# Performance work log

Hardware: AMD Instinct MI355X
Metric: run time of the kernel (lower is better)

Reference implementation:

```python
import jax, jax.numpy as jnp
import numpy as np
import math

D_MODEL = 1024
N_HEAD = 16
B, T = 4, 2048


def setup_inputs() -> dict:
    key = jax.random.key(0)
    ks = jax.random.split(key, 12)
    s = 1.0 / math.sqrt(D_MODEL)
    inp = {
        "q": jax.random.normal(ks[0], (B, T, D_MODEL), dtype=jnp.float32),
        "k": jax.random.normal(ks[1], (B, T, D_MODEL), dtype=jnp.float32),
        "v": jax.random.normal(ks[2], (B, T, D_MODEL), dtype=jnp.float32),
        "Wq": jax.random.uniform(ks[3], (D_MODEL, D_MODEL), jnp.float32, -s, s),
        "bq": jax.random.uniform(ks[4], (D_MODEL,), jnp.float32, -s, s),
        "Wk": jax.random.uniform(ks[5], (D_MODEL, D_MODEL), jnp.float32, -s, s),
        "bk": jax.random.uniform(ks[6], (D_MODEL,), jnp.float32, -s, s),
        "Wv": jax.random.uniform(ks[7], (D_MODEL, D_MODEL), jnp.float32, -s, s),
        "bv": jax.random.uniform(ks[8], (D_MODEL,), jnp.float32, -s, s),
        "Wo": jax.random.uniform(ks[9], (D_MODEL, D_MODEL), jnp.float32, -s, s),
        "bo": jax.random.uniform(ks[10], (D_MODEL,), jnp.float32, -s, s),
    }
    return inp


def reference(q, k, v, Wq, bq, Wk, bk, Wv, bv, Wo, bo):
    # NOTE: original module applies all three projections to `q` (k, v args unused)
    batch, time, dim = q.shape
    n_d = dim // N_HEAD
    # torch Linear: x @ W.T + b
    Q = (q @ Wq.T + bq).reshape(batch, time, N_HEAD, n_d).transpose(0, 2, 1, 3)
    K = (q @ Wk.T + bk).reshape(batch, time, N_HEAD, n_d).transpose(0, 2, 1, 3)
    V = (q @ Wv.T + bv).reshape(batch, time, N_HEAD, n_d).transpose(0, 2, 1, 3)
    # [B, H, T, T]
    score = jnp.einsum("bhqd,bhkd->bhqk", Q, K) / jnp.sqrt(jnp.float32(n_d))
    causal = jnp.tril(jnp.ones((time, time), dtype=bool))
    score = jnp.where(causal, score, -jnp.inf)
    # original uses Softmax(dim=-2): normalizes over the QUERY axis (faithful)
    attn = jax.nn.softmax(score, axis=-2)
    ctx = jnp.einsum("bhqk,bhkd->bhqd", attn, V)
    ctx = ctx.transpose(0, 2, 1, 3).reshape(batch, time, dim)
    return ctx @ Wo.T + bo
```

## Files before the change

### kernel.cpp

```cpp
#include <hip/hip_runtime.h>
#include <hip/hip_bf16.h>
#include <cstdint>
#include <cstddef>

typedef __bf16 bf16x8 __attribute__((ext_vector_type(8)));
typedef __bf16 bf16x4 __attribute__((ext_vector_type(4)));
typedef __bf16 bf16x2 __attribute__((ext_vector_type(2)));
typedef float  f32x4  __attribute__((ext_vector_type(4)));

static constexpr int TSEQ  = 2048;
static constexpr int DM    = 1024;
static constexpr int NH    = 16;
static constexpr int HD    = 64;
static constexpr int BATCH = 4;
static constexpr float SCL = 0.18033688011112042f;

__device__ __forceinline__ void gload16(const __bf16* g, __bf16* l) {
  __builtin_amdgcn_global_load_lds((const __attribute__((address_space(1))) void*)g,
                                   (__attribute__((address_space(3))) void*)l, 16, 0, 0);
}

#define PBAR()  asm volatile("s_barrier" ::: "memory")
#define LGKM()  asm volatile("s_waitcnt lgkmcnt(0)" ::: "memory")

__global__ __launch_bounds__(256) void cvt_kernel(const float* __restrict__ in,
                                                  __bf16* __restrict__ out, int n4) {
  int i = blockIdx.x * 256 + threadIdx.x;
  if (i < n4) {
    float4 v = reinterpret_cast<const float4*>(in)[i];
    bf16x4 o;
    o[0] = (__bf16)v.x; o[1] = (__bf16)v.y; o[2] = (__bf16)v.z; o[3] = (__bf16)v.w;
    reinterpret_cast<bf16x4*>(out)[i] = o;
  }
}

__global__ __launch_bounds__(256) void cvt4_kernel(
    const float* __restrict__ a, const float* __restrict__ bsrc,
    const float* __restrict__ c, const float* __restrict__ d,
    __bf16* __restrict__ oa, __bf16* __restrict__ ob,
    __bf16* __restrict__ oc, __bf16* __restrict__ od, int n4) {
  const float* src = (blockIdx.y == 0) ? a : (blockIdx.y == 1) ? bsrc
                    : (blockIdx.y == 2) ? c : d;
  __bf16* dst = (blockIdx.y == 0) ? oa : (blockIdx.y == 1) ? ob
               : (blockIdx.y == 2) ? oc : od;
  int i = blockIdx.x * 256 + threadIdx.x;
  if (i < n4) {
    float4 v = reinterpret_cast<const float4*>(src)[i];
    bf16x4 o;
    o[0] = (__bf16)v.x; o[1] = (__bf16)v.y; o[2] = (__bf16)v.z; o[3] = (__bf16)v.w;
    reinterpret_cast<bf16x4*>(dst)[i] = o;
  }
}

__global__ __launch_bounds__(512, 2) void gemm_qkv_kernel(
    const __bf16* __restrict__ A, const __bf16* __restrict__ Wqkv,
    const float* __restrict__ b0, const float* __restrict__ b1,
    const float* __restrict__ b2, __bf16* __restrict__ QKVp) {
  __shared__ __align__(16) __bf16 lA[2 * 256 * 64];
  __shared__ __align__(16) __bf16 lB[2 * 192 * 64];
  const int flat = blockIdx.x;
  const int xcd = flat & 7, idx = flat >> 3;
  const int mi = xcd * 4 + (idx & 3);
  const int nig = idx >> 2;
  const int i0 = mi * 256, o0 = nig * 192;

  const int tid = threadIdx.x;
  const int l = tid & 63, lr = l & 15, lg = l >> 4;
  const int w = tid >> 6;
  const int wr = w >> 2, wc = w & 3;

  f32x4 acc[8][3];
  const f32x4 fzero = {0.f, 0.f, 0.f, 0.f};
#pragma unroll
  for (int mm = 0; mm < 8; ++mm)
#pragma unroll
    for (int ni = 0; ni < 3; ++ni) acc[mm][ni] = fzero;

  const int s_row = tid >> 3;
  const int s_cc  = tid & 7;
  const __bf16* Ab = A + (size_t)i0 * DM;
  const __bf16* Wb = Wqkv + (size_t)o0 * DM;

  auto stageA = [&](int buf, int kt, int h) {
#pragma unroll
    for (int rr = 0; rr < 2; ++rr) {
      int row = h * 128 + rr * 64 + s_row;
      gload16(Ab + (size_t)row * DM + kt * 64 + ((s_cc ^ (row & 7)) << 3),
              lA + buf * 16384 + (h * 128 + rr * 64) * 64 + tid * 8);
    }
  };
  auto stageB = [&](int buf, int kt, int n) {
    int row = n * 64 + s_row;
    gload16(Wb + (size_t)row * DM + kt * 64 + ((s_cc ^ (row & 7)) << 3),
            lB + buf * 12288 + n * 4096 + tid * 8);
  };
  auto rdA = [&](const __bf16* base, int row, int ks) {
    int chunk = (ks * 4 + lg) ^ (row & 7);
    return *(const bf16x8*)(base + row * 64 + chunk * 8);
  };

  const int NT = DM / 64;

#pragma unroll
  for (int h = 0; h < 2; ++h) stageA(0, 0, h);
#pragma unroll
  for (int n = 0; n < 3; ++n) stageB(0, 0, n);
#pragma unroll
  for (int h = 0; h < 2; ++h) stageA(1, 1, h);
#pragma unroll
  for (int n = 0; n < 3; ++n) stageB(1, 1, n);
  asm volatile("s_waitcnt vmcnt(7)" ::: "memory");
  PBAR();

  for (int t = 0; t < NT; ++t) {
    const int cur = t & 1;
    const __bf16* cA = lA + cur * 16384;
    const __bf16* cB = lB + cur * 12288;
    const bool pre = (t + 2 < NT);

    bf16x8 afl[4][2], afh[4][2], bfl[2][2], bfh[1][2];

#pragma unroll
    for (int mm = 0; mm < 4; ++mm)
#pragma unroll
      for (int ks = 0; ks < 2; ++ks)
        afl[mm][ks] = rdA(cA, wr * 128 + mm * 16 + lr, ks);
#pragma unroll
    for (int ni = 0; ni < 2; ++ni)
#pragma unroll
      for (int ks = 0; ks < 2; ++ks)
        bfl[ni][ks] = rdA(cB, wc * 48 + ni * 16 + lr, ks);
    PBAR(); LGKM();
    __builtin_amdgcn_s_setprio(1);
#pragma unroll
    for (int mm = 0; mm < 4; ++mm)
#pragma unroll
      for (int ni = 0; ni < 2; ++ni)
#pragma unroll
        for (int ks = 0; ks < 2; ++ks)
          acc[mm][ni] = __builtin_amdgcn_mfma_f32_16x16x32_bf16(
              afl[mm][ks], bfl[ni][ks], acc[mm][ni], 0, 0, 0);
    __builtin_amdgcn_s_setprio(0);
    PBAR();

#pragma unroll
    for (int ks = 0; ks < 2; ++ks)
      bfh[0][ks] = rdA(cB, wc * 48 + 2 * 16 + lr, ks);
    if (pre) { stageB(cur, t + 2, 0); stageB(cur, t + 2, 1); }
    PBAR(); LGKM();
    __builtin_amdgcn_s_setprio(1);
#pragma unroll
    for (int mm = 0; mm < 4; ++mm)
#pragma unroll
      for (int ks = 0; ks < 2; ++ks)
        acc[mm][2] = __builtin_amdgcn_mfma_f32_16x16x32_bf16(
            afl[mm][ks], bfh[0][ks], acc[mm][2], 0, 0, 0);
    __builtin_amdgcn_s_setprio(0);
    PBAR();

#pragma unroll
    for (int mm = 0; mm < 4; ++mm)
#pragma unroll
      for (int ks = 0; ks < 2; ++ks)
        afh[mm][ks] = rdA(cA, wr * 128 + (mm + 4) * 16 + lr, ks);
    if (pre) { stageB(cur, t + 2, 2); stageA(cur, t + 2, 0); }
    PBAR(); LGKM();
    __builtin_amdgcn_s_setprio(1);
#pragma unroll
    for (int mm = 0; mm < 4; ++mm)
#pragma unroll
      for (int ni = 0; ni < 2; ++ni)
#pragma unroll
        for (int ks = 0; ks < 2; ++ks)
          acc[mm + 4][ni] = __builtin_amdgcn_mfma_f32_16x16x32_bf16(
              afh[mm][ks], bfl[ni][ks], acc[mm + 4][ni], 0, 0, 0);
    __builtin_amdgcn_s_setprio(0);
    PBAR();

    if (pre) stageA(cur, t + 2, 1);
    if (pre)                asm volatile("s_waitcnt vmcnt(7)" ::: "memory");
    else if (t + 1 < NT)    asm volatile("s_waitcnt vmcnt(0)" ::: "memory");
    PBAR();
    __builtin_amdgcn_s_setprio(1);
#pragma unroll
    for (int mm = 0; mm < 4; ++mm)
#pragma unroll
      for (int ks = 0; ks < 2; ++ks)
        acc[mm + 4][2] = __builtin_amdgcn_mfma_f32_16x16x32_bf16(
            afh[mm][ks], bfh[0][ks], acc[mm + 4][2], 0, 0, 0);
    __builtin_amdgcn_s_setprio(0);
    PBAR();
  }

#pragma unroll
  for (int ni = 0; ni < 3; ++ni) {
    int col = o0 + wc * 48 + ni * 16 + lr;
    int z = col >> 10, cin = col & 1023;
    const float* bp = (z == 0) ? b0 : (z == 1) ? b1 : b2;
    float bb = bp[cin];
    __bf16* O = QKVp + (size_t)z * 8192 * DM;
#pragma unroll
    for (int mm = 0; mm < 8; ++mm) {
      int row = i0 + wr * 128 + mm * 16 + lg * 4;
#pragma unroll
      for (int r = 0; r < 4; ++r)
        O[(size_t)(row + r) * DM + cin] = (__bf16)(acc[mm][ni][r] + bb);
    }
  }
}

template <typename OUT_T>
__device__ __forceinline__ void gemm_body2(
    const __bf16* __restrict__ A, const __bf16* __restrict__ W,
    const float* __restrict__ bias, OUT_T* __restrict__ C,
    int i0, int o0, __bf16* lA, __bf16* lB) {
  const int tid = threadIdx.x;
  const int l = tid & 63, lr = l & 15, lg = l >> 4;
  const int w = tid >> 6;
  const int wr = w >> 2, wc = w & 3;

  f32x4 acc[4][4];
  const f32x4 fzero = {0.f, 0.f, 0.f, 0.f};
#pragma unroll
  for (int mi = 0; mi < 4; ++mi)
#pragma unroll
    for (int ni = 0; ni < 4; ++ni) acc[mi][ni] = fzero;

  const int s_row = tid >> 3;
  const int s_cc  = tid & 7;
  const int NT = DM / 64;

  {
#pragma unroll
    for (int n = 0; n < 2; ++n) {
      int row = n * 64 + s_row;
      gload16(A + (size_t)(i0 + row) * DM + ((s_cc ^ (row & 7)) << 3),
              lA + n * 4096 + tid * 8);
    }
#pragma unroll
    for (int n = 0; n < 4; ++n) {
      int row = n * 64 + s_row;
      gload16(W + (size_t)(o0 + row) * DM + ((s_cc ^ (row & 7)) << 3),
              lB + n * 4096 + tid * 8);
    }
  }
  asm volatile("s_waitcnt vmcnt(0)" ::: "memory");
  __syncthreads();

  for (int t = 0; t < NT; ++t) {
    const int cur = t & 1;
    if (t + 1 < NT) {
      const int k0 = (t + 1) * 64;
      const int nxt = cur ^ 1;
#pragma unroll
      for (int n = 0; n < 2; ++n) {
        int row = n * 64 + s_row;
        gload16(A + (size_t)(i0 + row) * DM + k0 + ((s_cc ^ (row & 7)) << 3),
                lA + nxt * 8192 + n * 4096 + tid * 8);
      }
#pragma unroll
      for (int n = 0; n < 4; ++n) {
        int row = n * 64 + s_row;
        gload16(W + (size_t)(o0 + row) * DM + k0 + ((s_cc ^ (row & 7)) << 3),
                lB + nxt * 16384 + n * 4096 + tid * 8);
      }
    }

    const __bf16* cA = lA + cur * 8192;
    const __bf16* cB = lB + cur * 16384;

    bf16x8 af[4][2], bf_[2][2];
#pragma unroll
    for (int mi = 0; mi < 4; ++mi)
#pragma unroll
      for (int ks = 0; ks < 2; ++ks) {
        int row = wr * 64 + mi * 16 + lr;
        int chunk = (ks * 4 + lg) ^ (row & 7);
        af[mi][ks] = *(const bf16x8*)(cA + row * 64 + chunk * 8);
      }
#pragma unroll
    for (int ni = 0; ni < 2; ++ni)
#pragma unroll
      for (int ks = 0; ks < 2; ++ks) {
        int row = wc * 64 + ni * 16 + lr;
        int chunk = (ks * 4 + lg) ^ (row & 7);
        bf_[ni][ks] = *(const bf16x8*)(cB + row * 64 + chunk * 8);
      }
    __builtin_amdgcn_s_setprio(1);
#pragma unroll
    for (int mi = 0; mi < 4; ++mi)
#pragma unroll
      for (int ni = 0; ni < 2; ++ni)
#pragma unroll
        for (int ks = 0; ks < 2; ++ks)
          acc[mi][ni] = __builtin_amdgcn_mfma_f32_16x16x32_bf16(
              af[mi][ks], bf_[ni][ks], acc[mi][ni], 0, 0, 0);
    __builtin_amdgcn_s_setprio(0);

#pragma unroll
    for (int ni = 0; ni < 2; ++ni)
#pragma unroll
      for (int ks = 0; ks < 2; ++ks) {
        int row = wc * 64 + (ni + 2) * 16 + lr;
        int chunk = (ks * 4 + lg) ^ (row & 7);
        bf_[ni][ks] = *(const bf16x8*)(cB + row * 64 + chunk * 8);
      }
    __builtin_amdgcn_s_setprio(1);
#pragma unroll
    for (int mi = 0; mi < 4; ++mi)
#pragma unroll
      for (int ni = 0; ni < 2; ++ni)
#pragma unroll
        for (int ks = 0; ks < 2; ++ks)
          acc[mi][ni + 2] = __builtin_amdgcn_mfma_f32_16x16x32_bf16(
              af[mi][ks], bf_[ni][ks], acc[mi][ni + 2], 0, 0, 0);
    __builtin_amdgcn_s_setprio(0);

    if (t + 1 < NT) {
      asm volatile("s_waitcnt vmcnt(0)" ::: "memory");
      __syncthreads();
    }
  }

#pragma unroll
  for (int ni = 0; ni < 4; ++ni) {
    int col = o0 + wc * 64 + ni * 16 + lr;
    float bb = bias[col];
#pragma unroll
    for (int mi = 0; mi < 4; ++mi) {
      int row = i0 + wr * 64 + mi * 16 + lg * 4;
#pragma unroll
      for (int r = 0; r < 4; ++r)
        C[(size_t)(row + r) * DM + col] = (OUT_T)(acc[mi][ni][r] + bb);
    }
  }
}

__global__ __launch_bounds__(512, 2) void gemm_out_kernel(
    const __bf16* __restrict__ A, const __bf16* __restrict__ W,
    const float* __restrict__ bias, float* __restrict__ C) {
  __shared__ __align__(16) __bf16 lA[2 * 128 * 64];
  __shared__ __align__(16) __bf16 lB[2 * 256 * 64];
  const int flat = blockIdx.x;
  const int xcd = flat & 7, idx = flat >> 3;
  const int mi = xcd * 8 + (idx & 7);
  const int ni = idx >> 3;
  gemm_body2<float>(A, W, bias, C, mi * 128, ni * 256, lA, lB);
}

__global__ __launch_bounds__(256) void colstats_kernel(
    const __bf16* __restrict__ Q, const __bf16* __restrict__ K,
    const __bf16* __restrict__ V, __bf16* __restrict__ VT) {
  const int flat = blockIdx.x;
  const int wid = (flat & 7) * 128 + (flat >> 3);
  const int g = wid >> 4, bx = wid & 15;
  const int h = g & 15, b = g >> 4;
  const int tid = threadIdx.x;
  const int w = tid >> 6, l = tid & 63, lr = l & 15, lg = l >> 4;
  const size_t base = (size_t)b * TSEQ * DM + (size_t)h * HD;

  __shared__ float part[4][64];
  __shared__ float invc[64];

  for (int ph = 0; ph < 2; ++ph) {
    const int kt = ph ? (31 - bx) : bx;
    const int k0 = kt * 64;

    bf16x8 kf[4][2];
#pragma unroll
    for (int ct = 0; ct < 4; ++ct)
#pragma unroll
      for (int ks = 0; ks < 2; ++ks)
        kf[ct][ks] = *(const bf16x8*)(K + base + (size_t)(k0 + ct * 16 + lr) * DM +
                                      ks * 32 + lg * 8);

    float csum[4] = {0.f, 0.f, 0.f, 0.f};
    const int nchunks = (TSEQ - k0) >> 4;
    for (int jj = w; jj < nchunks; jj += 4) {
      int qrow = k0 + jj * 16;
      bf16x8 a0 = *(const bf16x8*)(Q + base + (size_t)(qrow + lr) * DM + lg * 8);
      bf16x8 a1 = *(const bf16x8*)(Q + base + (size_t)(qrow + lr) * DM + 32 + lg * 8);
      const bool interior = (jj >= 4);
#pragma unroll
      for (int ct = 0; ct < 4; ++ct) {
        f32x4 s = {0.f, 0.f, 0.f, 0.f};
        s = __builtin_amdgcn_mfma_f32_16x16x32_bf16(a0, kf[ct][0], s, 0, 0, 0);
        s = __builtin_amdgcn_mfma_f32_16x16x32_bf16(a1, kf[ct][1], s, 0, 0, 0);
        if (interior) {
#pragma unroll
          for (int r = 0; r < 4; ++r) csum[ct] += __builtin_amdgcn_exp2f(s[r] * SCL);
        } else {
#pragma unroll
          for (int r = 0; r < 4; ++r) {
            int ql = jj * 16 + lg * 4 + r;
            int kl = ct * 16 + lr;
            float e = __builtin_amdgcn_exp2f(s[r] * SCL);
            csum[ct] += (ql >= kl) ? e : 0.f;
          }
        }
      }
    }

#pragma unroll
    for (int ct = 0; ct < 4; ++ct) {
      csum[ct] += __shfl_xor(csum[ct], 16, 64);
      csum[ct] += __shfl_xor(csum[ct], 32, 64);
    }

    if (l < 16) {
#pragma unroll
      for (int ct = 0; ct < 4; ++ct) part[w][ct * 16 + l] = csum[ct];
    }
    __syncthreads();
    if (tid < 64) {
      float c = part[0][tid] + part[1][tid] + part[2][tid] + part[3][tid];
      invc[tid] = 1.0f / c;
    }
    __syncthreads();

    const int d = tid >> 2, gq = tid & 3;
    size_t vtb = (((size_t)(b * NH + h)) * HD + d) * TSEQ + k0 + gq * 16;
#pragma unroll
    for (int kc = 0; kc < 16; kc += 2) {
      int kl = gq * 16 + kc;
      float v0 = (float)V[base + (size_t)(k0 + kl) * DM + d] * invc[kl];
      float v1 = (float)V[base + (size_t)(k0 + kl + 1) * DM + d] * invc[kl + 1];
      bf16x2 o; o[0] = (__bf16)v0; o[1] = (__bf16)v1;
      *(bf16x2*)(VT + vtb + kc) = o;
    }
    __syncthreads();
  }
}

__device__ __forceinline__ int swz(int e) { return e ^ (((e >> 6) & 7) << 3); }

__global__ __launch_bounds__(256, 4) void ctx_kernel(
    const __bf16* __restrict__ Q, const __bf16* __restrict__ K,
    const __bf16* __restrict__ VT, __bf16* __restrict__ CTX) {
  __shared__ __align__(16) __bf16 lK[4096];
  __shared__ __align__(16) __bf16 lV[4096];
  __shared__ __align__(16) __bf16 lP[8][16 * 88];
  const int flat = blockIdx.x;
  const int wid = (flat & 7) * 128 + (flat >> 3);
  const int g = wid >> 4, bx = wid & 15;
  const int h = g & 15, b = g >> 4;
  const int tid = threadIdx.x;
  const int w = tid >> 6, l = tid & 63, lr = l & 15, lg = l >> 4;
  const size_t base = (size_t)b * TSEQ * DM + (size_t)h * HD;
  const size_t vtb = ((size_t)(b * NH + h)) * HD * TSEQ;
  __bf16* pw1 = &lP[w][0];
  __bf16* pw2 = &lP[w + 4][0];

  const int qt1 = 31 - bx, qt2 = bx;
  const int q01 = qt1 * 64, q02 = qt2 * 64;

  const int srow = w * 8 + (l >> 3);
  const int scol = (((l & 7) ^ (l >> 3)) << 3);

  bf16x8 qf1[2], qf2[2];
#pragma unroll
  for (int ks = 0; ks < 2; ++ks) {
    qf1[ks] = *(const bf16x8*)(Q + base + (size_t)(q01 + w * 16 + lr) * DM + ks * 32 + lg * 8);
    qf2[ks] = *(const bf16x8*)(Q + base + (size_t)(q02 + w * 16 + lr) * DM + ks * 32 + lg * 8);
  }

  f32x4 acc1[4], acc2[4];
  const f32x4 fzero = {0.f, 0.f, 0.f, 0.f};
#pragma unroll
  for (int dt = 0; dt < 4; ++dt) { acc1[dt] = fzero; acc2[dt] = fzero; }

  for (int kt = 0; kt <= qt1; ++kt) {
    const int k0 = kt * 64;
    const bool two = (kt <= qt2);
    __syncthreads();
#pragma unroll
    for (int n = 0; n < 2; ++n) {
      gload16(K + base + (size_t)(k0 + n * 32 + srow) * DM + scol,
              lK + n * 2048 + w * 512);
      gload16(VT + vtb + (size_t)(n * 32 + srow) * TSEQ + k0 + scol,
              lV + n * 2048 + w * 512);
    }
    asm volatile("s_waitcnt vmcnt(0)" ::: "memory");
    __syncthreads();

    const bool diag1 = (kt == qt1), diag2 = (kt == qt2);
#pragma unroll
    for (int ct = 0; ct < 4; ++ct) {
      bf16x8 kb[2];
#pragma unroll
      for (int ks = 0; ks < 2; ++ks) {
        int e = (ct * 16 + lr) * 64 + ks * 32 + lg * 8;
        kb[ks] = *(const bf16x8*)(lK + swz(e));
      }
      {
        f32x4 s = {0.f, 0.f, 0.f, 0.f};
        s = __builtin_amdgcn_mfma_f32_16x16x32_bf16(kb[0], qf1[0], s, 0, 0, 0);
        s = __builtin_amdgcn_mfma_f32_16x16x32_bf16(kb[1], qf1[1], s, 0, 0, 0);
        bf16x4 pk;
        if (diag1) {
#pragma unroll
          for (int r = 0; r < 4; ++r) {
            int ql = w * 16 + lr, kl = ct * 16 + lg * 4 + r;
            pk[r] = (__bf16)((ql >= kl) ? __builtin_amdgcn_exp2f(s[r] * SCL) : 0.f);
          }
        } else {
#pragma unroll
          for (int r = 0; r < 4; ++r)
            pk[r] = (__bf16)__builtin_amdgcn_exp2f(s[r] * SCL);
        }
        *(bf16x4*)(pw1 + lr * 88 + ct * 16 + lg * 4) = pk;
      }
      if (two) {
        f32x4 s = {0.f, 0.f, 0.f, 0.f};
        s = __builtin_amdgcn_mfma_f32_16x16x32_bf16(kb[0], qf2[0], s, 0, 0, 0);
        s = __builtin_amdgcn_mfma_f32_16x16x32_bf16(kb[1], qf2[1], s, 0, 0, 0);
        bf16x4 pk;
        if (diag2) {
#pragma unroll
          for (int r = 0; r < 4; ++r) {
            int ql = w * 16 + lr, kl = ct * 16 + lg * 4 + r;
            pk[r] = (__bf16)((ql >= kl) ? __builtin_amdgcn_exp2f(s[r] * SCL) : 0.f);
          }
        } else {
#pragma unroll
          for (int r = 0; r < 4; ++r)
            pk[r] = (__bf16)__builtin_amdgcn_exp2f(s[r] * SCL);
        }
        *(bf16x4*)(pw2 + lr * 88 + ct * 16 + lg * 4) = pk;
      }
    }
    asm volatile("" ::: "memory");

    bf16x8 pa1[2], pa2[2];
#pragma unroll
    for (int ks = 0; ks < 2; ++ks)
      pa1[ks] = *(const bf16x8*)(pw1 + lr * 88 + ks * 32 + lg * 8);
    if (two) {
#pragma unroll
      for (int ks = 0; ks < 2; ++ks)
        pa2[ks] = *(const bf16x8*)(pw2 + lr * 88 + ks * 32 + lg * 8);
    }
#pragma unroll
    for (int dt = 0; dt < 4; ++dt) {
#pragma unroll
      for (int ks = 0; ks < 2; ++ks) {
        int e = (dt * 16 + lr) * 64 + ks * 32 + lg * 8;
        bf16x8 vb8 = *(const bf16x8*)(lV + swz(e));
        acc1[dt] = __builtin_amdgcn_mfma_f32_16x16x32_bf16(pa1[ks], vb8, acc1[dt], 0, 0, 0);
        if (two)
          acc2[dt] = __builtin_amdgcn_mfma_f32_16x16x32_bf16(pa2[ks], vb8, acc2[dt], 0, 0, 0);
      }
    }
  }

#pragma unroll
  for (int dt = 0; dt < 4; ++dt)
#pragma unroll
    for (int r = 0; r < 4; ++r) {
      CTX[base + (size_t)(q01 + w * 16 + lg * 4 + r) * DM + dt * 16 + lr] = (__bf16)acc1[dt][r];
      CTX[base + (size_t)(q02 + w * 16 + lg * 4 + r) * DM + dt * 16 + lr] = (__bf16)acc2[dt][r];
    }
}

extern "C" void kernel_launch(void* const* d_in, const int* in_sizes, int n_in,
                              void* d_out, int out_size, void* d_ws, size_t ws_size,
                              hipStream_t stream) {
  const float* q  = (const float*)d_in[0];
  const float* Wq = (const float*)d_in[3];
  const float* bq = (const float*)d_in[4];
  const float* Wk = (const float*)d_in[5];
  const float* bk = (const float*)d_in[6];
  const float* Wv = (const float*)d_in[7];
  const float* bv = (const float*)d_in[8];
  const float* Wo = (const float*)d_in[9];
  const float* bo = (const float*)d_in[10];
  float* out = (float*)d_out;

  const size_t NTOK = (size_t)BATCH * TSEQ;
  char* ws = (char*)d_ws;
  __bf16* qb   = (__bf16*)ws; ws += NTOK * DM * 2;
  __bf16* Wqkv = (__bf16*)ws; ws += 3 * (size_t)DM * DM * 2;
  __bf16* Wob  = (__bf16*)ws; ws += (size_t)DM * DM * 2;
  __bf16* QKVp = (__bf16*)ws; ws += 3 * NTOK * DM * 2;
  __bf16* VT   = (__bf16*)ws; ws += (size_t)BATCH * NH * HD * TSEQ * 2;
  __bf16* CTX = qb;

  __bf16* Qp = QKVp;
  __bf16* Kp = QKVp + NTOK * DM;
  __bf16* Vp = QKVp + 2 * NTOK * DM;

  const int nq4 = (int)(NTOK * DM / 4);
  const int nw4 = DM * DM / 4;
  cvt_kernel<<<(nq4 + 255) / 256, 256, 0, stream>>>(q, qb, nq4);
  cvt4_kernel<<<dim3((nw4 + 255) / 256, 4), 256, 0, stream>>>(
      Wq, Wk, Wv, Wo, Wqkv, Wqkv + (size_t)DM * DM, Wqkv + 2 * (size_t)DM * DM, Wob, nw4);

  gemm_qkv_kernel<<<512, 512, 0, stream>>>(qb, Wqkv, bq, bk, bv, QKVp);

  colstats_kernel<<<1024, 256, 0, stream>>>(Qp, Kp, Vp, VT);
  ctx_kernel<<<1024, 256, 0, stream>>>(Qp, Kp, VT, CTX);

  gemm_out_kernel<<<256, 512, 0, stream>>>(CTX, Wob, bo, out);
}
```

Measured before the change: 209.1 us.

## Prefetch next-tile LDS fragments in QKV GEMM and fuse colstats key-tile phases

The QKV GEMM main loop now loads the next tile's A/B low fragments from LDS at the end of each iteration, and moves the afh loads earlier. It uses partial lgkmcnt waits so LDS reads overlap with MFMA work instead of stalling at full waits. The colstats kernel handles both key tiles (bx and 31-bx) in one pass over Q rows, so each Q fragment is loaded once and shared by both tiles' score sums. This costs more registers (two K fragment sets, persistent fragment arrays) and could reduce occupancy.

```diff
diff --git a/kernel.cpp b/kernel.cpp
--- a/kernel.cpp
+++ b/kernel.cpp
@@ -20,8 +20,8 @@
                                    (__attribute__((address_space(3))) void*)l, 16, 0, 0);
 }
 
-#define PBAR()  asm volatile("s_barrier" ::: "memory")
-#define LGKM()  asm volatile("s_waitcnt lgkmcnt(0)" ::: "memory")
+#define PBAR()   asm volatile("s_barrier" ::: "memory")
+#define LGKMN(n) asm volatile("s_waitcnt lgkmcnt(" #n ")" ::: "memory")
 
 __global__ __launch_bounds__(256) void cvt_kernel(const float* __restrict__ in,
                                                   __bf16* __restrict__ out, int n4) {
@@ -112,25 +112,31 @@
   asm volatile("s_waitcnt vmcnt(7)" ::: "memory");
   PBAR();
 
+  bf16x8 afl[4][2], afh[4][2], bfl[2][2], bfh[2];
+#pragma unroll
+  for (int mm = 0; mm < 4; ++mm)
+#pragma unroll
+    for (int ks = 0; ks < 2; ++ks)
+      afl[mm][ks] = rdA(lA, wr * 128 + mm * 16 + lr, ks);
+#pragma unroll
+  for (int ni = 0; ni < 2; ++ni)
+#pragma unroll
+    for (int ks = 0; ks < 2; ++ks)
+      bfl[ni][ks] = rdA(lB, wc * 48 + ni * 16 + lr, ks);
+
   for (int t = 0; t < NT; ++t) {
     const int cur = t & 1;
     const __bf16* cA = lA + cur * 16384;
     const __bf16* cB = lB + cur * 12288;
+    const __bf16* nA = lA + (cur ^ 1) * 16384;
+    const __bf16* nB = lB + (cur ^ 1) * 12288;
     const bool pre = (t + 2 < NT);
-
-    bf16x8 afl[4][2], afh[4][2], bfl[2][2], bfh[1][2];
-
-#pragma unroll
-    for (int mm = 0; mm < 4; ++mm)
-#pragma unroll
-      for (int ks = 0; ks < 2; ++ks)
-        afl[mm][ks] = rdA(cA, wr * 128 + mm * 16 + lr, ks);
-#pragma unroll
-    for (int ni = 0; ni < 2; ++ni)
-#pragma unroll
-      for (int ks = 0; ks < 2; ++ks)
-        bfl[ni][ks] = rdA(cB, wc * 48 + ni * 16 + lr, ks);
-    PBAR(); LGKM();
+    const bool hasnext = (t + 1 < NT);
+
+#pragma unroll
+    for (int ks = 0; ks < 2; ++ks)
+      bfh[ks] = rdA(cB, wc * 48 + 2 * 16 + lr, ks);
+    PBAR(); LGKMN(2);
     __builtin_amdgcn_s_setprio(1);
 #pragma unroll
     for (int mm = 0; mm < 4; ++mm)
@@ -144,27 +150,24 @@
     PBAR();
 
 #pragma unroll
-    for (int ks = 0; ks < 2; ++ks)
-      bfh[0][ks] = rdA(cB, wc * 48 + 2 * 16 + lr, ks);
+    for (int mm = 0; mm < 4; ++mm)
+#pragma unroll
+      for (int ks = 0; ks < 2; ++ks)
+        afh[mm][ks] = rdA(cA, wr * 128 + (mm + 4) * 16 + lr, ks);
     if (pre) { stageB(cur, t + 2, 0); stageB(cur, t + 2, 1); }
-    PBAR(); LGKM();
+    PBAR(); LGKMN(8);
     __builtin_amdgcn_s_setprio(1);
 #pragma unroll
     for (int mm = 0; mm < 4; ++mm)
 #pragma unroll
       for (int ks = 0; ks < 2; ++ks)
         acc[mm][2] = __builtin_amdgcn_mfma_f32_16x16x32_bf16(
-            afl[mm][ks], bfh[0][ks], acc[mm][2], 0, 0, 0);
+            afl[mm][ks], bfh[ks], acc[mm][2], 0, 0, 0);
     __builtin_amdgcn_s_setprio(0);
     PBAR();
 
-#pragma unroll
-    for (int mm = 0; mm < 4; ++mm)
-#pragma unroll
-      for (int ks = 0; ks < 2; ++ks)
-        afh[mm][ks] = rdA(cA, wr * 128 + (mm + 4) * 16 + lr, ks);
     if (pre) { stageB(cur, t + 2, 2); stageA(cur, t + 2, 0); }
-    PBAR(); LGKM();
+    PBAR(); LGKMN(0);
     __builtin_amdgcn_s_setprio(1);
 #pragma unroll
     for (int mm = 0; mm < 4; ++mm)
@@ -179,15 +182,27 @@
 
     if (pre) stageA(cur, t + 2, 1);
     if (pre)                asm volatile("s_waitcnt vmcnt(7)" ::: "memory");
-    else if (t + 1 < NT)    asm volatile("s_waitcnt vmcnt(0)" ::: "memory");
+    else if (hasnext)       asm volatile("s_waitcnt vmcnt(0)" ::: "memory");
     PBAR();
+    if (hasnext) {
+#pragma unroll
+      for (int mm = 0; mm < 4; ++mm)
+#pragma unroll
+        for (int ks = 0; ks < 2; ++ks)
+          afl[mm][ks] = rdA(nA, wr * 128 + mm * 16 + lr, ks);
+#pragma unroll
+      for (int ni = 0; ni < 2; ++ni)
+#pragma unroll
+        for (int ks = 0; ks < 2; ++ks)
+          bfl[ni][ks] = rdA(nB, wc * 48 + ni * 16 + lr, ks);
+    }
     __builtin_amdgcn_s_setprio(1);
 #pragma unroll
     for (int mm = 0; mm < 4; ++mm)
 #pragma unroll
       for (int ks = 0; ks < 2; ++ks)
         acc[mm + 4][2] = __builtin_amdgcn_mfma_f32_16x16x32_bf16(
-            afh[mm][ks], bfh[0][ks], acc[mm + 4][2], 0, 0, 0);
+            afh[mm][ks], bfh[ks], acc[mm + 4][2], 0, 0, 0);
     __builtin_amdgcn_s_setprio(0);
     PBAR();
   }
@@ -359,76 +374,122 @@
   const int w = tid >> 6, l = tid & 63, lr = l & 15, lg = l >> 4;
   const size_t base = (size_t)b * TSEQ * DM + (size_t)h * HD;
 
+  const int kt1 = 31 - bx, kt2 = bx;
+  const int k01 = kt1 * 64, k02 = kt2 * 64;
+
   __shared__ float part[4][64];
   __shared__ float invc[64];
 
-  for (int ph = 0; ph < 2; ++ph) {
-    const int kt = ph ? (31 - bx) : bx;
-    const int k0 = kt * 64;
-
-    bf16x8 kf[4][2];
-#pragma unroll
-    for (int ct = 0; ct < 4; ++ct)
-#pragma unroll
-      for (int ks = 0; ks < 2; ++ks)
-        kf[ct][ks] = *(const bf16x8*)(K + base + (size_t)(k0 + ct * 16 + lr) * DM +
-                                      ks * 32 + lg * 8);
-
-    float csum[4] = {0.f, 0.f, 0.f, 0.f};
-    const int nchunks = (TSEQ - k0) >> 4;
-    for (int jj = w; jj < nchunks; jj += 4) {
-      int qrow = k0 + jj * 16;
-      bf16x8 a0 = *(const bf16x8*)(Q + base + (size_t)(qrow + lr) * DM + lg * 8);
-      bf16x8 a1 = *(const bf16x8*)(Q + base + (size_t)(qrow + lr) * DM + 32 + lg * 8);
+  bf16x8 kf1[4][2], kf2[4][2];
+#pragma unroll
+  for (int ct = 0; ct < 4; ++ct)
+#pragma unroll
+    for (int ks = 0; ks < 2; ++ks) {
+      kf1[ct][ks] = *(const bf16x8*)(K + base + (size_t)(k01 + ct * 16 + lr) * DM +
+                                     ks * 32 + lg * 8);
+      kf2[ct][ks] = *(const bf16x8*)(K + base + (size_t)(k02 + ct * 16 + lr) * DM +
+                                     ks * 32 + lg * 8);
+    }
+
+  float csum1[4] = {0.f, 0.f, 0.f, 0.f};
+  float csum2[4] = {0.f, 0.f, 0.f, 0.f};
+  const int nchunks = (TSEQ - k02) >> 4;
+  for (int jj = w; jj < nchunks; jj += 4) {
+    const int qrow = k02 + jj * 16;
+    bf16x8 a0 = *(const bf16x8*)(Q + base + (size_t)(qrow + lr) * DM + lg * 8);
+    bf16x8 a1 = *(const bf16x8*)(Q + base + (size_t)(qrow + lr) * DM + 32 + lg * 8);
+
+    {
       const bool interior = (jj >= 4);
 #pragma unroll
       for (int ct = 0; ct < 4; ++ct) {
         f32x4 s = {0.f, 0.f, 0.f, 0.f};
-        s = __builtin_amdgcn_mfma_f32_16x16x32_bf16(a0, kf[ct][0], s, 0, 0, 0);
-        s = __builtin_amdgcn_mfma_f32_16x16x32_bf16(a1, kf[ct][1], s, 0, 0, 0);
+        s = __builtin_amdgcn_mfma_f32_16x16x32_bf16(a0, kf2[ct][0], s, 0, 0, 0);
+        s = __builtin_amdgcn_mfma_f32_16x16x32_bf16(a1, kf2[ct][1], s, 0, 0, 0);
         if (interior) {
 #pragma unroll
-          for (int r = 0; r < 4; ++r) csum[ct] += __builtin_amdgcn_exp2f(s[r] * SCL);
+          for (int r = 0; r < 4; ++r) csum2[ct] += __builtin_amdgcn_exp2f(s[r] * SCL);
         } else {
 #pragma unroll
           for (int r = 0; r < 4; ++r) {
             int ql = jj * 16 + lg * 4 + r;
             int kl = ct * 16 + lr;
             float e = __builtin_amdgcn_exp2f(s[r] * SCL);
-            csum[ct] += (ql >= kl) ? e : 0.f;
+            csum2[ct] += (ql >= kl) ? e : 0.f;
           }
         }
       }
     }
-
-#pragma unroll
-    for (int ct = 0; ct < 4; ++ct) {
-      csum[ct] += __shfl_xor(csum[ct], 16, 64);
-      csum[ct] += __shfl_xor(csum[ct], 32, 64);
-    }
-
-    if (l < 16) {
-#pragma unroll
-      for (int ct = 0; ct < 4; ++ct) part[w][ct * 16 + l] = csum[ct];
-    }
-    __syncthreads();
-    if (tid < 64) {
-      float c = part[0][tid] + part[1][tid] + part[2][tid] + part[3][tid];
-      invc[tid] = 1.0f / c;
-    }
-    __syncthreads();
-
-    const int d = tid >> 2, gq = tid & 3;
-    size_t vtb = (((size_t)(b * NH + h)) * HD + d) * TSEQ + k0 + gq * 16;
+    if (qrow >= k01) {
+      const bool interior = (qrow >= k01 + 64);
+#pragma unroll
+      for (int ct = 0; ct < 4; ++ct) {
+        f32x4 s = {0.f, 0.f, 0.f, 0.f};
+        s = __builtin_amdgcn_mfma_f32_16x16x32_bf16(a0, kf1[ct][0], s, 0, 0, 0);
+        s = __builtin_amdgcn_mfma_f32_16x16x32_bf16(a1, kf1[ct][1], s, 0, 0, 0);
+        if (interior) {
+#pragma unroll
+          for (int r = 0; r < 4; ++r) csum1[ct] += __builtin_amdgcn_exp2f(s[r] * SCL);
+        } else {
+#pragma unroll
+          for (int r = 0; r < 4; ++r) {
+            int ql = (qrow - k01) + lg * 4 + r;
+            int kl = ct * 16 + lr;
+            float e = __builtin_amdgcn_exp2f(s[r] * SCL);
+            csum1[ct] += (ql >= kl) ? e : 0.f;
+          }
+        }
+      }
+    }
+  }
+
+#pragma unroll
+  for (int ct = 0; ct < 4; ++ct) {
+    csum1[ct] += __shfl_xor(csum1[ct], 16, 64);
+    csum1[ct] += __shfl_xor(csum1[ct], 32, 64);
+    csum2[ct] += __shfl_xor(csum2[ct], 16, 64);
+    csum2[ct] += __shfl_xor(csum2[ct], 32, 64);
+  }
+
+  const int d = tid >> 2, gq = tid & 3;
+  if (l < 16) {
+#pragma unroll
+    for (int ct = 0; ct < 4; ++ct) part[w][ct * 16 + l] = csum1[ct];
+  }
+  __syncthreads();
+  if (tid < 64)
+    invc[tid] = 1.0f / (part[0][tid] + part[1][tid] + part[2][tid] + part[3][tid]);
+  __syncthreads();
+  {
+    size_t vtb = (((size_t)(b * NH + h)) * HD + d) * TSEQ + k01 + gq * 16;
 #pragma unroll
     for (int kc = 0; kc < 16; kc += 2) {
       int kl = gq * 16 + kc;
-      float v0 = (float)V[base + (size_t)(k0 + kl) * DM + d] * invc[kl];
-      float v1 = (float)V[base + (size_t)(k0 + kl + 1) * DM + d] * invc[kl + 1];
+      float v0 = (float)V[base + (size_t)(k01 + kl) * DM + d] * invc[kl];
+      float v1 = (float)V[base + (size_t)(k01 + kl + 1) * DM + d] * invc[kl + 1];
       bf16x2 o; o[0] = (__bf16)v0; o[1] = (__bf16)v1;
       *(bf16x2*)(VT + vtb + kc) = o;
     }
-    __syncthreads();
+  }
+  __syncthreads();
+  if (l < 16) {
+#pragma unroll
+    for (int ct = 0; ct < 4; ++ct) part[w][ct * 16 + l] = csum2[ct];
+  }
+  __syncthreads();
+  if (tid < 64)
+    invc[tid] = 1.0f / (part[0][tid] + part[1][tid] + part[2][tid] + part[3][tid]);
+  __syncthreads();
+  {
+    size_t vtb = (((size_t)(b * NH + h)) * HD + d) * TSEQ + k02 + gq * 16;
+#pragma unroll
+    for (int kc = 0; kc < 16; kc += 2) {
+      int kl = gq * 16 + kc;
+      float v0 = (float)V[base + (size_t)(k02 + kl) * DM + d] * invc[kl];
+      float v1 = (float)V[base + (size_t)(k02 + kl + 1) * DM + d] * invc[kl + 1];
+      bf16x2 o; o[0] = (__bf16)v0; o[1] = (__bf16)v1;
+      *(bf16x2*)(VT + vtb + kc) = o;
+    }
   }
 }
 
```

After: 209.0 us. About the same (-0.0%).
